# Kernel tuning notes

Measured on AMD Instinct MI355X. Metric: run time of the kernel, lower is better.

## Reference

```python
import jax, jax.numpy as jnp
import numpy as np

NEG_FILL = -10000000.0  # matches torch masked_fill value


def setup_inputs() -> dict:
    key = jax.random.key(0)
    kq, kk, kv = jax.random.split(key, 3)
    B, H, S, D = 4, 16, 2048, 64
    Q = jax.random.normal(kq, (B, H, S, D), dtype=jnp.float32)
    K = jax.random.normal(kk, (B, H, S, D), dtype=jnp.float32)
    V = jax.random.normal(kv, (B, H, S, D), dtype=jnp.float32)
    return {"Q": Q, "K": K, "V": V}


def reference(Q, K, V):
    # Q,K,V: [B,H,S,D]
    D = K.shape[-1]
    scale = 1.0 / jnp.sqrt(jnp.asarray(D, dtype=Q.dtype))
    # scores: [B,H,S,S]
    scores = jnp.einsum("bhqd,bhkd->bhqk", Q, K) * scale
    S = scores.shape[-1]
    # causal mask: True above diagonal (future positions) -> filled with NEG_FILL
    causal = jnp.triu(jnp.ones((S, S), dtype=bool), k=1)
    scores = jnp.where(causal, jnp.asarray(NEG_FILL, dtype=scores.dtype), scores)
    attn = jax.nn.softmax(scores, axis=-1)
    return jnp.einsum("bhqk,bhkd->bhqd", attn, V)
```

## Files before the change

kernel.cpp:

```cpp
#include <hip/hip_runtime.h>
#include <hip/hip_bf16.h>


#define SEQ 2048
#define DIM 64
#define BH  64

typedef _Float16 half8  __attribute__((ext_vector_type(8)));
typedef _Float16 half4v __attribute__((ext_vector_type(4)));
typedef float    float4v __attribute__((ext_vector_type(4)));
typedef unsigned short ushort4v __attribute__((ext_vector_type(4)));

__device__ __forceinline__ void async16(const _Float16* g, _Float16* l) {
    __builtin_amdgcn_global_load_lds(
        (const __attribute__((address_space(1))) void*)g,
        (__attribute__((address_space(3))) void*)l, 16, 0, 0);
}

#if defined(__has_builtin)
#if __has_builtin(__builtin_elementwise_min)
#define EMIN4(a, b) __builtin_elementwise_min((a), (b))
#endif
#if __has_builtin(__builtin_amdgcn_exp2f)
#define EXP2F(x) __builtin_amdgcn_exp2f(x)
#endif
#endif
#ifndef EMIN4
__device__ __forceinline__ half4v emin4_fallback(half4v a, half4v b) {
    half4v r;
    r[0] = a[0] < b[0] ? a[0] : b[0];
    r[1] = a[1] < b[1] ? a[1] : b[1];
    r[2] = a[2] < b[2] ? a[2] : b[2];
    r[3] = a[3] < b[3] ? a[3] : b[3];
    return r;
}
#define EMIN4(a, b) emin4_fallback((a), (b))
#endif
#ifndef EXP2F
#define EXP2F(x) exp2f(x)
#endif

__global__ __launch_bounds__(256)
void prep_kernel(const float* __restrict__ K, const float* __restrict__ V,
                 _Float16* __restrict__ Kh, _Float16* __restrict__ Vt) {
    const int bid = blockIdx.x;
    const int tid = threadIdx.x;
    if (bid < 4096) {
        size_t idx = (size_t)bid * 2048 + (size_t)tid * 8;
        float4v a = *(const float4v*)(K + idx);
        float4v b = *(const float4v*)(K + idx + 4);
        half8 h;
        h[0] = (_Float16)a[0]; h[1] = (_Float16)a[1];
        h[2] = (_Float16)a[2]; h[3] = (_Float16)a[3];
        h[4] = (_Float16)b[0]; h[5] = (_Float16)b[1];
        h[6] = (_Float16)b[2]; h[7] = (_Float16)b[3];
        *(half8*)(Kh + idx) = h;
    } else {
        __shared__ _Float16 Vl[64 * 64];
        const int b  = bid - 4096;
        const int bh = b >> 5;
        const int s0 = (b & 31) * 64;
        {
            const int r   = tid >> 2;
            const int c16 = (tid & 3) * 16;
            const float* p = V + ((size_t)bh * SEQ + s0 + r) * DIM + c16;
            float4v x0 = *(const float4v*)(p);
            float4v x1 = *(const float4v*)(p + 4);
            float4v x2 = *(const float4v*)(p + 8);
            float4v x3 = *(const float4v*)(p + 12);
            half8 h0, h1;
            h0[0] = (_Float16)x0[0]; h0[1] = (_Float16)x0[1];
            h0[2] = (_Float16)x0[2]; h0[3] = (_Float16)x0[3];
            h0[4] = (_Float16)x1[0]; h0[5] = (_Float16)x1[1];
            h0[6] = (_Float16)x1[2]; h0[7] = (_Float16)x1[3];
            h1[0] = (_Float16)x2[0]; h1[1] = (_Float16)x2[1];
            h1[2] = (_Float16)x2[2]; h1[3] = (_Float16)x2[3];
            h1[4] = (_Float16)x3[0]; h1[5] = (_Float16)x3[1];
            h1[6] = (_Float16)x3[2]; h1[7] = (_Float16)x3[3];
            const int k  = (r + (r >> 3)) & 7;
            const int j0 = c16 >> 3;
            *(half8*)&Vl[r * 64 + ((j0    ) ^ k) * 8] = h0;
            *(half8*)&Vl[r * 64 + ((j0 + 1) ^ k) * 8] = h1;
        }
        __syncthreads();
        {
            const int d  = tid >> 2;
            const int sc = (tid & 3) * 16;
            const int dh = d >> 3;
            const int dl = d & 7;
            half8 o0, o1;
#pragma unroll
            for (int j = 0; j < 8; ++j) {
                const int s1 = sc + j;
                const int s2 = sc + 8 + j;
                o0[j] = Vl[s1 * 64 + ((dh ^ ((s1 + (s1 >> 3)) & 7)) << 3) + dl];
                o1[j] = Vl[s2 * 64 + ((dh ^ ((s2 + (s2 >> 3)) & 7)) << 3) + dl];
            }
            _Float16* op = Vt + ((size_t)bh * DIM + d) * SEQ + s0 + sc;
            *(half8*)op       = o0;
            *(half8*)(op + 8) = o1;
        }
    }
}

__global__ __launch_bounds__(128, 2)
void fa_main(const float* __restrict__ Q, const _Float16* __restrict__ Kh,
             const _Float16* __restrict__ Vt, float* __restrict__ O) {
    const int bid = blockIdx.x;
    const int xcd = bid & 7;
    const int idx = bid >> 3;
    const int bh  = xcd * 8 + (idx & 7);
    const int t   = 31 - (idx >> 3);

    const float*    Qb = Q  + (size_t)bh * SEQ * DIM;
    const _Float16* Kb = Kh + (size_t)bh * SEQ * DIM;
    const _Float16* Vb = Vt + (size_t)bh * DIM * SEQ;
    float*          Ob = O  + (size_t)bh * SEQ * DIM;

    const int tid  = threadIdx.x;
    const int wave = tid >> 6;
    const int lane = tid & 63;
    const int row  = lane & 15;
    const int quad = lane >> 4;

    __shared__ _Float16 Kl[2][64 * 64];
    __shared__ _Float16 Vl[64 * 64];
    __shared__ _Float16 Pl[2][32 * 64];

    const float SC = 0.125f * 1.44269504f;
    const float4v z0 = {0.f, 0.f, 0.f, 0.f};
    half8 ones;
    {
        ushort4v ob;
        ob[0] = 0x3c00; ob[1] = 0x3c00; ob[2] = 0x3c00; ob[3] = 0x3c00;
        half4v o1 = __builtin_bit_cast(half4v, ob);
        ones[0] = o1[0]; ones[1] = o1[1]; ones[2] = o1[2]; ones[3] = o1[3];
        ones[4] = o1[0]; ones[5] = o1[1]; ones[6] = o1[2]; ones[7] = o1[3];
    }
    half4v wcap;
    {
        ushort4v cb2;
        cb2[0] = 0x7400; cb2[1] = 0x7400; cb2[2] = 0x7400; cb2[3] = 0x7400;
        wcap = __builtin_bit_cast(half4v, cb2);
    }

#define STAGE_K(bsel, kt_)                                                      \
    {                                                                           \
        const _Float16* Kt0 = Kb + (size_t)(kt_) * 64 * DIM;                    \
        _Pragma("unroll")                                                       \
        for (int i = 0; i < 4; ++i) {                                           \
            int pos = wave * 256 + i * 64 + lane;                               \
            int rr  = pos >> 3;                                                 \
            int cc  = (pos & 7) ^ (rr & 7);                                     \
            async16(Kt0 + (size_t)rr * DIM + cc * 8,                            \
                    &Kl[bsel][0] + (size_t)(wave * 256 + i * 64) * 8);          \
        }                                                                       \
    }
#define STAGE_V(kt_)                                                            \
    {                                                                           \
        const _Float16* Vt0 = Vb + (size_t)(kt_) * 64;                          \
        _Pragma("unroll")                                                       \
        for (int i = 0; i < 4; ++i) {                                           \
            int pos = wave * 256 + i * 64 + lane;                               \
            int rr  = pos >> 3;                                                 \
            int cc  = (pos & 7) ^ (rr & 7);                                     \
            async16(Vt0 + (size_t)rr * SEQ + cc * 8,                            \
                    &Vl[0] + (size_t)(wave * 256 + i * 64) * 8);                \
        }                                                                       \
    }

    const int q0 = t * 64;

    half8 qf[4];
#pragma unroll
    for (int qs = 0; qs < 2; ++qs) {
        const float* qp = Qb + (size_t)(q0 + wave * 32 + qs * 16 + row) * DIM;
#pragma unroll
        for (int s = 0; s < 2; ++s) {
            const float* p = qp + s * 32 + quad * 8;
            float4v a = *(const float4v*)p;
            float4v b = *(const float4v*)(p + 4);
            half8 h;
            h[0] = (_Float16)(a[0] * SC); h[1] = (_Float16)(a[1] * SC);
            h[2] = (_Float16)(a[2] * SC); h[3] = (_Float16)(a[3] * SC);
            h[4] = (_Float16)(b[0] * SC); h[5] = (_Float16)(b[1] * SC);
            h[6] = (_Float16)(b[2] * SC); h[7] = (_Float16)(b[3] * SC);
            qf[qs * 2 + s] = h;
        }
    }

    float4v o_acc[2][4];
    float4v lacc[2];
#pragma unroll
    for (int qs = 0; qs < 2; ++qs) {
        float4v z = {0.f, 0.f, 0.f, 0.f};
        lacc[qs] = z;
#pragma unroll
        for (int c = 0; c < 4; ++c) o_acc[qs][c] = z;
    }

    STAGE_K(0, 0)
    __syncthreads();

    for (int kt = 0; kt <= t; ++kt) {
        const int cb = kt & 1;
        STAGE_V(kt)
        if (kt < t) STAGE_K(cb ^ 1, kt + 1)

        float4v sacc[2][4];
        __builtin_amdgcn_s_setprio(1);
#pragma unroll
        for (int c = 0; c < 4; ++c) {
            const int kv  = c * 16 + row;
            const int ch0 = quad ^ (row & 7);
            const int ch1 = (4 + quad) ^ (row & 7);
            half8 kf0 = *(const half8*)&Kl[cb][kv * 64 + ch0 * 8];
            half8 kf1 = *(const half8*)&Kl[cb][kv * 64 + ch1 * 8];
#pragma unroll
            for (int qs = 0; qs < 2; ++qs) {
                float4v s0 = __builtin_amdgcn_mfma_f32_16x16x32_f16(kf0, qf[qs * 2 + 0], z0, 0, 0, 0);
                sacc[qs][c] = __builtin_amdgcn_mfma_f32_16x16x32_f16(kf1, qf[qs * 2 + 1], s0, 0, 0, 0);
            }
        }
        __builtin_amdgcn_s_setprio(0);

        float pv[2][4][4];
        if (kt == t) {
#pragma unroll
            for (int qs = 0; qs < 2; ++qs) {
                const int ql = wave * 32 + qs * 16 + row;
#pragma unroll
                for (int c = 0; c < 4; ++c)
#pragma unroll
                    for (int rr = 0; rr < 4; ++rr) {
                        int kvl = c * 16 + quad * 4 + rr;
                        float sx = (kvl > ql) ? -1e30f : sacc[qs][c][rr];
                        pv[qs][c][rr] = EXP2F(sx);
                    }
            }
        } else {
#pragma unroll
            for (int qs = 0; qs < 2; ++qs)
#pragma unroll
                for (int c = 0; c < 4; ++c)
#pragma unroll
                    for (int rr = 0; rr < 4; ++rr)
                        pv[qs][c][rr] = EXP2F(sacc[qs][c][rr]);
        }

#pragma unroll
        for (int qs = 0; qs < 2; ++qs)
#pragma unroll
            for (int c = 0; c < 4; ++c) {
#if defined(__has_builtin) && __has_builtin(__builtin_amdgcn_cvt_pkrtz)
                auto t0 = __builtin_amdgcn_cvt_pkrtz(pv[qs][c][0], pv[qs][c][1]);
                auto t1 = __builtin_amdgcn_cvt_pkrtz(pv[qs][c][2], pv[qs][c][3]);
                half4v w;
                w[0] = t0[0]; w[1] = t0[1]; w[2] = t1[0]; w[3] = t1[1];
#else
                half4v w;
                w[0] = (_Float16)pv[qs][c][0]; w[1] = (_Float16)pv[qs][c][1];
                w[2] = (_Float16)pv[qs][c][2]; w[3] = (_Float16)pv[qs][c][3];
#endif
                w = EMIN4(w, wcap);
                const int jc  = c * 2 + (quad >> 1);
                const int col = ((jc ^ (row & 7)) << 3) + (quad & 1) * 4;
                *(half4v*)&Pl[wave][(qs * 16 + row) * 64 + col] = w;
            }
        asm volatile("s_waitcnt lgkmcnt(0)" ::: "memory");
        half8 af[2][2];
#pragma unroll
        for (int qs = 0; qs < 2; ++qs)
#pragma unroll
            for (int s = 0; s < 2; ++s) {
                const int js = (s * 4 + quad) ^ (row & 7);
                af[qs][s] = *(const half8*)&Pl[wave][(qs * 16 + row) * 64 + js * 8];
            }

        if (kt < t) {
            asm volatile("s_waitcnt vmcnt(4)" ::: "memory");
        } else {
            asm volatile("s_waitcnt vmcnt(0)" ::: "memory");
        }
        __builtin_amdgcn_s_barrier();
        __builtin_amdgcn_sched_barrier(0);

        __builtin_amdgcn_s_setprio(1);
#pragma unroll
        for (int c = 0; c < 4; ++c) {
            const int d = c * 16 + row;
#pragma unroll
            for (int s = 0; s < 2; ++s) {
                const int ch = (s * 4 + quad) ^ (row & 7);
                half8 vf = *(const half8*)&Vl[d * 64 + ch * 8];
                o_acc[0][c] = __builtin_amdgcn_mfma_f32_16x16x32_f16(vf, af[0][s], o_acc[0][c], 0, 0, 0);
                o_acc[1][c] = __builtin_amdgcn_mfma_f32_16x16x32_f16(vf, af[1][s], o_acc[1][c], 0, 0, 0);
            }
        }
#pragma unroll
        for (int qs = 0; qs < 2; ++qs)
#pragma unroll
            for (int s = 0; s < 2; ++s)
                lacc[qs] = __builtin_amdgcn_mfma_f32_16x16x32_f16(ones, af[qs][s], lacc[qs], 0, 0, 0);
        __builtin_amdgcn_s_setprio(0);

        __syncthreads();
    }

#pragma unroll
    for (int qs = 0; qs < 2; ++qs) {
        const float inv = 1.0f / lacc[qs][0];
        float* op = Ob + (size_t)(q0 + wave * 32 + qs * 16 + row) * DIM + quad * 4;
#pragma unroll
        for (int c = 0; c < 4; ++c) {
            float4v o;
            o[0] = o_acc[qs][c][0] * inv; o[1] = o_acc[qs][c][1] * inv;
            o[2] = o_acc[qs][c][2] * inv; o[3] = o_acc[qs][c][3] * inv;
            *(float4v*)(op + c * 16) = o;
        }
    }
}

__global__ __launch_bounds__(256)
void fa_causal_fallback(const float* __restrict__ Q, const float* __restrict__ K,
                        const float* __restrict__ V, float* __restrict__ O) {
    const int bid = blockIdx.x;
    const int bh  = bid >> 5;
    const int qt  = bid & 31;
    const int q0  = qt * 64;

    const float* Qb = Q + (size_t)bh * SEQ * DIM;
    const float* Kb = K + (size_t)bh * SEQ * DIM;
    const float* Vb = V + (size_t)bh * SEQ * DIM;
    float*       Ob = O + (size_t)bh * SEQ * DIM;

    const int tid  = threadIdx.x;
    const int wave = tid >> 6;
    const int lane = tid & 63;
    const int row  = lane & 15;
    const int quad = lane >> 4;

    __shared__ _Float16 Kl[64][72];
    __shared__ _Float16 Vt[64][72];
    __shared__ _Float16 Pl[4][16][72];

    half8 qf[2];
    {
        const float* qp = Qb + (size_t)(q0 + wave * 16 + row) * DIM;
#pragma unroll
        for (int s = 0; s < 2; ++s) {
            const float* p = qp + s * 32 + quad * 8;
            float4v a = *(const float4v*)p;
            float4v b = *(const float4v*)(p + 4);
            half8 h;
            h[0] = (_Float16)a[0]; h[1] = (_Float16)a[1];
            h[2] = (_Float16)a[2]; h[3] = (_Float16)a[3];
            h[4] = (_Float16)b[0]; h[5] = (_Float16)b[1];
            h[6] = (_Float16)b[2]; h[7] = (_Float16)b[3];
            qf[s] = h;
        }
    }

    float m_i[4] = {-1e30f, -1e30f, -1e30f, -1e30f};
    float l_i[4] = {0.f, 0.f, 0.f, 0.f};
    float4v o_acc[4];
#pragma unroll
    for (int c = 0; c < 4; ++c) { float4v z = {0.f, 0.f, 0.f, 0.f}; o_acc[c] = z; }

    const float LOG2E = 1.44269504f;

    for (int kt = 0; kt <= qt; ++kt) {
        __syncthreads();
        {
            const int kvr = tid >> 2;
            const int c4  = tid & 3;
            const float* kp = Kb + (size_t)(kt * 64 + kvr) * DIM + c4 * 16;
            const float* vp = Vb + (size_t)(kt * 64 + kvr) * DIM + c4 * 16;
#pragma unroll
            for (int i = 0; i < 4; ++i) {
                float4v kx = *(const float4v*)(kp + i * 4);
                float4v vx = *(const float4v*)(vp + i * 4);
#pragma unroll
                for (int j = 0; j < 4; ++j) {
                    Kl[kvr][c4 * 16 + i * 4 + j] = (_Float16)kx[j];
                    Vt[c4 * 16 + i * 4 + j][kvr] = (_Float16)vx[j];
                }
            }
        }
        __syncthreads();

        float4v sacc[4];
#pragma unroll
        for (int c = 0; c < 4; ++c) { float4v z = {0.f, 0.f, 0.f, 0.f}; sacc[c] = z; }
#pragma unroll
        for (int c = 0; c < 4; ++c)
#pragma unroll
            for (int s = 0; s < 2; ++s) {
                half8 kf = *(const half8*)&Kl[c * 16 + row][s * 32 + quad * 8];
                sacc[c] = __builtin_amdgcn_mfma_f32_16x16x32_f16(qf[s], kf, sacc[c], 0, 0, 0);
            }

        float sv[4][4];
        const bool diag = (kt == qt);
#pragma unroll
        for (int c = 0; c < 4; ++c)
#pragma unroll
            for (int r = 0; r < 4; ++r) {
                float v = sacc[c][r] * 0.125f;
                if (diag) {
                    int kvl = c * 16 + row;
                    int ql  = wave * 16 + quad * 4 + r;
                    if (kvl > ql) v = -1e30f;
                }
                sv[c][r] = v;
            }

        float mnew[4], alpha[4];
#pragma unroll
        for (int r = 0; r < 4; ++r) {
            float rm = fmaxf(fmaxf(sv[0][r], sv[1][r]), fmaxf(sv[2][r], sv[3][r]));
            rm = fmaxf(rm, __shfl_xor(rm, 1));
            rm = fmaxf(rm, __shfl_xor(rm, 2));
            rm = fmaxf(rm, __shfl_xor(rm, 4));
            rm = fmaxf(rm, __shfl_xor(rm, 8));
            mnew[r]  = fmaxf(m_i[r], rm);
            alpha[r] = exp2f((m_i[r] - mnew[r]) * LOG2E);
            m_i[r]   = mnew[r];
        }
        float rs[4] = {0.f, 0.f, 0.f, 0.f};
#pragma unroll
        for (int c = 0; c < 4; ++c)
#pragma unroll
            for (int r = 0; r < 4; ++r) {
                float p = exp2f((sv[c][r] - mnew[r]) * LOG2E);
                sv[c][r] = p;
                rs[r] += p;
            }
#pragma unroll
        for (int r = 0; r < 4; ++r) {
            float s = rs[r];
            s += __shfl_xor(s, 1);
            s += __shfl_xor(s, 2);
            s += __shfl_xor(s, 4);
            s += __shfl_xor(s, 8);
            l_i[r] = l_i[r] * alpha[r] + s;
        }
#pragma unroll
        for (int c = 0; c < 4; ++c)
#pragma unroll
            for (int r = 0; r < 4; ++r)
                o_acc[c][r] *= alpha[r];

#pragma unroll
        for (int c = 0; c < 4; ++c)
#pragma unroll
            for (int r = 0; r < 4; ++r)
                Pl[wave][quad * 4 + r][c * 16 + row] = (_Float16)sv[c][r];
        __syncthreads();

        half8 af[2];
#pragma unroll
        for (int s = 0; s < 2; ++s)
            af[s] = *(const half8*)&Pl[wave][row][s * 32 + quad * 8];
#pragma unroll
        for (int c = 0; c < 4; ++c)
#pragma unroll
            for (int s = 0; s < 2; ++s) {
                half8 vf = *(const half8*)&Vt[c * 16 + row][s * 32 + quad * 8];
                o_acc[c] = __builtin_amdgcn_mfma_f32_16x16x32_f16(af[s], vf, o_acc[c], 0, 0, 0);
            }
    }

#pragma unroll
    for (int r = 0; r < 4; ++r) {
        float inv = 1.0f / l_i[r];
        float* op = Ob + (size_t)(q0 + wave * 16 + quad * 4 + r) * DIM;
#pragma unroll
        for (int c = 0; c < 4; ++c)
            op[c * 16 + row] = o_acc[c][r] * inv;
    }
}

extern "C" void kernel_launch(void* const* d_in, const int* in_sizes, int n_in,
                              void* d_out, int out_size, void* d_ws, size_t ws_size,
                              hipStream_t stream) {
    const float* Q = (const float*)d_in[0];
    const float* K = (const float*)d_in[1];
    const float* V = (const float*)d_in[2];
    float* O = (float*)d_out;

    const size_t elems = (size_t)BH * SEQ * DIM;
    const size_t need  = 2 * elems * sizeof(_Float16);

    if (ws_size >= need) {
        _Float16* Kh = (_Float16*)d_ws;
        _Float16* Vt = Kh + elems;
        prep_kernel<<<4096 + 2048, 256, 0, stream>>>(K, V, Kh, Vt);
        fa_main<<<BH * 32, 128, 0, stream>>>(Q, Kh, Vt, O);
    } else {
        fa_causal_fallback<<<BH * 32, 256, 0, stream>>>(Q, K, V, O);
    }
}
```

Before: 184.7 us.

## Use single-wave blocks with 32x32 tiles and barrier-free software pipeline

Shrinks each attention block to one wavefront covering 32 queries, with 32-key K/V tiles. The grid doubles to 4096 blocks. Block-wide barriers are replaced by explicit vmcnt waits around a prefetch schedule that stages the next V and the next-but-one K tile after the PV step. The diagonal tile gets its own specialized iteration. This is meant to remove barrier stalls, shrink shared memory for higher occupancy, and cut wasted causal work at finer granularity. The cost is that K/V tiles are no longer shared between two waves, so global/L2 traffic per query roughly doubles.

```diff
diff --git a/kernel.cpp b/kernel.cpp
--- a/kernel.cpp
+++ b/kernel.cpp
@@ -103,29 +103,27 @@
     }
 }
 
-__global__ __launch_bounds__(128, 2)
+__global__ __launch_bounds__(64, 2)
 void fa_main(const float* __restrict__ Q, const _Float16* __restrict__ Kh,
              const _Float16* __restrict__ Vt, float* __restrict__ O) {
     const int bid = blockIdx.x;
     const int xcd = bid & 7;
     const int idx = bid >> 3;
     const int bh  = xcd * 8 + (idx & 7);
-    const int t   = 31 - (idx >> 3);
+    const int t   = 63 - (idx >> 3);
 
     const float*    Qb = Q  + (size_t)bh * SEQ * DIM;
     const _Float16* Kb = Kh + (size_t)bh * SEQ * DIM;
     const _Float16* Vb = Vt + (size_t)bh * DIM * SEQ;
     float*          Ob = O  + (size_t)bh * SEQ * DIM;
 
-    const int tid  = threadIdx.x;
-    const int wave = tid >> 6;
-    const int lane = tid & 63;
+    const int lane = threadIdx.x;
     const int row  = lane & 15;
     const int quad = lane >> 4;
 
-    __shared__ _Float16 Kl[2][64 * 64];
-    __shared__ _Float16 Vl[64 * 64];
-    __shared__ _Float16 Pl[2][32 * 64];
+    __shared__ _Float16 Kl[2][32 * 64];
+    __shared__ _Float16 Vl[64 * 32];
+    __shared__ _Float16 Pl[32 * 64];
 
     const float SC = 0.125f * 1.44269504f;
     const float4v z0 = {0.f, 0.f, 0.f, 0.f};
@@ -146,35 +144,35 @@
 
 #define STAGE_K(bsel, kt_)                                                      \
     {                                                                           \
-        const _Float16* Kt0 = Kb + (size_t)(kt_) * 64 * DIM;                    \
+        const _Float16* Kt0 = Kb + (size_t)(kt_) * 32 * DIM;                    \
         _Pragma("unroll")                                                       \
         for (int i = 0; i < 4; ++i) {                                           \
-            int pos = wave * 256 + i * 64 + lane;                               \
+            int pos = i * 64 + lane;                                            \
             int rr  = pos >> 3;                                                 \
             int cc  = (pos & 7) ^ (rr & 7);                                     \
             async16(Kt0 + (size_t)rr * DIM + cc * 8,                            \
-                    &Kl[bsel][0] + (size_t)(wave * 256 + i * 64) * 8);          \
+                    &Kl[bsel][0] + (size_t)pos * 8);                            \
         }                                                                       \
     }
 #define STAGE_V(kt_)                                                            \
     {                                                                           \
-        const _Float16* Vt0 = Vb + (size_t)(kt_) * 64;                          \
+        const _Float16* Vt0 = Vb + (size_t)(kt_) * 32;                          \
         _Pragma("unroll")                                                       \
         for (int i = 0; i < 4; ++i) {                                           \
-            int pos = wave * 256 + i * 64 + lane;                               \
-            int rr  = pos >> 3;                                                 \
-            int cc  = (pos & 7) ^ (rr & 7);                                     \
+            int pos = i * 64 + lane;                                            \
+            int rr  = pos >> 2;                                                 \
+            int cc  = (pos & 3) ^ (rr & 3);                                     \
             async16(Vt0 + (size_t)rr * SEQ + cc * 8,                            \
-                    &Vl[0] + (size_t)(wave * 256 + i * 64) * 8);                \
-        }                                                                       \
-    }
-
-    const int q0 = t * 64;
+                    &Vl[0] + (size_t)pos * 8);                                  \
+        }                                                                       \
+    }
+
+    const int q0 = t * 32;
 
     half8 qf[4];
 #pragma unroll
     for (int qs = 0; qs < 2; ++qs) {
-        const float* qp = Qb + (size_t)(q0 + wave * 32 + qs * 16 + row) * DIM;
+        const float* qp = Qb + (size_t)(q0 + qs * 16 + row) * DIM;
 #pragma unroll
         for (int s = 0; s < 2; ++s) {
             const float* p = qp + s * 32 + quad * 8;
@@ -200,117 +198,106 @@
     }
 
     STAGE_K(0, 0)
-    __syncthreads();
-
-    for (int kt = 0; kt <= t; ++kt) {
-        const int cb = kt & 1;
-        STAGE_V(kt)
-        if (kt < t) STAGE_K(cb ^ 1, kt + 1)
-
-        float4v sacc[2][4];
-        __builtin_amdgcn_s_setprio(1);
-#pragma unroll
-        for (int c = 0; c < 4; ++c) {
-            const int kv  = c * 16 + row;
-            const int ch0 = quad ^ (row & 7);
-            const int ch1 = (4 + quad) ^ (row & 7);
-            half8 kf0 = *(const half8*)&Kl[cb][kv * 64 + ch0 * 8];
-            half8 kf1 = *(const half8*)&Kl[cb][kv * 64 + ch1 * 8];
-#pragma unroll
-            for (int qs = 0; qs < 2; ++qs) {
-                float4v s0 = __builtin_amdgcn_mfma_f32_16x16x32_f16(kf0, qf[qs * 2 + 0], z0, 0, 0, 0);
-                sacc[qs][c] = __builtin_amdgcn_mfma_f32_16x16x32_f16(kf1, qf[qs * 2 + 1], s0, 0, 0, 0);
-            }
-        }
-        __builtin_amdgcn_s_setprio(0);
-
-        float pv[2][4][4];
-        if (kt == t) {
-#pragma unroll
-            for (int qs = 0; qs < 2; ++qs) {
-                const int ql = wave * 32 + qs * 16 + row;
-#pragma unroll
-                for (int c = 0; c < 4; ++c)
-#pragma unroll
-                    for (int rr = 0; rr < 4; ++rr) {
-                        int kvl = c * 16 + quad * 4 + rr;
-                        float sx = (kvl > ql) ? -1e30f : sacc[qs][c][rr];
-                        pv[qs][c][rr] = EXP2F(sx);
-                    }
-            }
-        } else {
-#pragma unroll
-            for (int qs = 0; qs < 2; ++qs)
-#pragma unroll
-                for (int c = 0; c < 4; ++c)
-#pragma unroll
-                    for (int rr = 0; rr < 4; ++rr)
-                        pv[qs][c][rr] = EXP2F(sacc[qs][c][rr]);
-        }
-
-#pragma unroll
-        for (int qs = 0; qs < 2; ++qs)
-#pragma unroll
-            for (int c = 0; c < 4; ++c) {
-#if defined(__has_builtin) && __has_builtin(__builtin_amdgcn_cvt_pkrtz)
-                auto t0 = __builtin_amdgcn_cvt_pkrtz(pv[qs][c][0], pv[qs][c][1]);
-                auto t1 = __builtin_amdgcn_cvt_pkrtz(pv[qs][c][2], pv[qs][c][3]);
-                half4v w;
-                w[0] = t0[0]; w[1] = t0[1]; w[2] = t1[0]; w[3] = t1[1];
-#else
-                half4v w;
-                w[0] = (_Float16)pv[qs][c][0]; w[1] = (_Float16)pv[qs][c][1];
-                w[2] = (_Float16)pv[qs][c][2]; w[3] = (_Float16)pv[qs][c][3];
-#endif
-                w = EMIN4(w, wcap);
-                const int jc  = c * 2 + (quad >> 1);
-                const int col = ((jc ^ (row & 7)) << 3) + (quad & 1) * 4;
-                *(half4v*)&Pl[wave][(qs * 16 + row) * 64 + col] = w;
-            }
-        asm volatile("s_waitcnt lgkmcnt(0)" ::: "memory");
-        half8 af[2][2];
-#pragma unroll
-        for (int qs = 0; qs < 2; ++qs)
-#pragma unroll
-            for (int s = 0; s < 2; ++s) {
-                const int js = (s * 4 + quad) ^ (row & 7);
-                af[qs][s] = *(const half8*)&Pl[wave][(qs * 16 + row) * 64 + js * 8];
-            }
-
-        if (kt < t) {
-            asm volatile("s_waitcnt vmcnt(4)" ::: "memory");
-        } else {
-            asm volatile("s_waitcnt vmcnt(0)" ::: "memory");
-        }
-        __builtin_amdgcn_s_barrier();
-        __builtin_amdgcn_sched_barrier(0);
-
-        __builtin_amdgcn_s_setprio(1);
-#pragma unroll
-        for (int c = 0; c < 4; ++c) {
-            const int d = c * 16 + row;
-#pragma unroll
-            for (int s = 0; s < 2; ++s) {
-                const int ch = (s * 4 + quad) ^ (row & 7);
-                half8 vf = *(const half8*)&Vl[d * 64 + ch * 8];
-                o_acc[0][c] = __builtin_amdgcn_mfma_f32_16x16x32_f16(vf, af[0][s], o_acc[0][c], 0, 0, 0);
-                o_acc[1][c] = __builtin_amdgcn_mfma_f32_16x16x32_f16(vf, af[1][s], o_acc[1][c], 0, 0, 0);
-            }
-        }
-#pragma unroll
-        for (int qs = 0; qs < 2; ++qs)
-#pragma unroll
-            for (int s = 0; s < 2; ++s)
-                lacc[qs] = __builtin_amdgcn_mfma_f32_16x16x32_f16(ones, af[qs][s], lacc[qs], 0, 0, 0);
-        __builtin_amdgcn_s_setprio(0);
-
-        __syncthreads();
-    }
+    STAGE_V(0)
+    if (t >= 1) STAGE_K(1, 1)
+
+#define KV_ITER(kt_, DIAG, STV, STK)                                            \
+    {                                                                           \
+        const int cb = (kt_) & 1;                                               \
+        if (DIAG) { asm volatile("s_waitcnt vmcnt(4)" ::: "memory"); }          \
+        else      { asm volatile("s_waitcnt vmcnt(8)" ::: "memory"); }          \
+        __builtin_amdgcn_sched_barrier(0);                                      \
+                                           \
+        float4v sacc[2][2];                                                     \
+        __builtin_amdgcn_s_setprio(1);                                          \
+        _Pragma("unroll")                                                       \
+        for (int c = 0; c < 2; ++c) {                                           \
+            const int kv  = c * 16 + row;                                       \
+            const int ch0 = quad ^ (kv & 7);                                    \
+            const int ch1 = (4 + quad) ^ (kv & 7);                              \
+            half8 kf0 = *(const half8*)&Kl[cb][kv * 64 + ch0 * 8];              \
+            half8 kf1 = *(const half8*)&Kl[cb][kv * 64 + ch1 * 8];              \
+            _Pragma("unroll")                                                   \
+            for (int qs = 0; qs < 2; ++qs) {                                    \
+                float4v s0 = __builtin_amdgcn_mfma_f32_16x16x32_f16(            \
+                    kf0, qf[qs * 2 + 0], z0, 0, 0, 0);                          \
+                sacc[qs][c] = __builtin_amdgcn_mfma_f32_16x16x32_f16(           \
+                    kf1, qf[qs * 2 + 1], s0, 0, 0, 0);                          \
+            }                                                                   \
+        }                                                                       \
+        __builtin_amdgcn_s_setprio(0);                                          \
+                               \
+        _Pragma("unroll")                                                       \
+        for (int qs = 0; qs < 2; ++qs) {                                        \
+            const int ql = qs * 16 + row;                                       \
+            _Pragma("unroll")                                                   \
+            for (int c = 0; c < 2; ++c) {                                       \
+                float p0[4];                                                    \
+                _Pragma("unroll")                                               \
+                for (int rr = 0; rr < 4; ++rr) {                                \
+                    float sx = sacc[qs][c][rr];                                 \
+                    if (DIAG) {                                                 \
+                        int kvl = c * 16 + quad * 4 + rr;                       \
+                        sx = (kvl > ql) ? -1e30f : sx;                          \
+                    }                                                           \
+                    p0[rr] = EXP2F(sx);                                         \
+                }                                                               \
+                half4v w;                                                       \
+                {                                                               \
+                    auto t0_ = __builtin_amdgcn_cvt_pkrtz(p0[0], p0[1]);        \
+                    auto t1_ = __builtin_amdgcn_cvt_pkrtz(p0[2], p0[3]);        \
+                    w[0] = t0_[0]; w[1] = t0_[1]; w[2] = t1_[0]; w[3] = t1_[1]; \
+                }                                                               \
+                w = EMIN4(w, wcap);                                             \
+                const int jc  = c * 2 + (quad >> 1);                            \
+                const int col = ((jc ^ (row & 7)) << 3) + (quad & 1) * 4;       \
+                *(half4v*)&Pl[(qs * 16 + row) * 64 + col] = w;                  \
+            }                                                                   \
+        }                                                                       \
+        asm volatile("s_waitcnt lgkmcnt(0)" ::: "memory");                      \
+        half8 af[2];                                                            \
+        {                                                                       \
+            const int js = quad ^ (row & 7);                                    \
+            af[0] = *(const half8*)&Pl[(row) * 64 + js * 8];                    \
+            af[1] = *(const half8*)&Pl[(16 + row) * 64 + js * 8];               \
+        }                                                                       \
+                 \
+        if (DIAG) { asm volatile("s_waitcnt vmcnt(0)" ::: "memory"); }          \
+        else      { asm volatile("s_waitcnt vmcnt(4)" ::: "memory"); }          \
+        __builtin_amdgcn_sched_barrier(0);                                      \
+                                        \
+        __builtin_amdgcn_s_setprio(1);                                          \
+        _Pragma("unroll")                                                       \
+        for (int c = 0; c < 4; ++c) {                                           \
+            const int d  = c * 16 + row;                                        \
+            const int ch = quad ^ (d & 3);                                      \
+            half8 vf = *(const half8*)&Vl[d * 32 + ch * 8];                     \
+            o_acc[0][c] = __builtin_amdgcn_mfma_f32_16x16x32_f16(               \
+                vf, af[0], o_acc[0][c], 0, 0, 0);                               \
+            o_acc[1][c] = __builtin_amdgcn_mfma_f32_16x16x32_f16(               \
+                vf, af[1], o_acc[1][c], 0, 0, 0);                               \
+        }                                                                       \
+        lacc[0] = __builtin_amdgcn_mfma_f32_16x16x32_f16(ones, af[0], lacc[0], 0, 0, 0); \
+        lacc[1] = __builtin_amdgcn_mfma_f32_16x16x32_f16(ones, af[1], lacc[1], 0, 0, 0); \
+        __builtin_amdgcn_s_setprio(0);                                          \
+        if (!(DIAG)) {                                                          \
+               \
+            asm volatile("s_waitcnt lgkmcnt(0)" ::: "memory");                  \
+            __builtin_amdgcn_sched_barrier(0);                                  \
+            if (STV) STAGE_V((kt_) + 1)                                         \
+            if (STK) STAGE_K(cb, (kt_) + 2)                                     \
+        }                                                                       \
+    }
+
+    for (int kt = 0; kt < t; ++kt) {
+        KV_ITER(kt, false, true, (kt < t - 1))
+    }
+    KV_ITER(t, true, false, false)
 
 #pragma unroll
     for (int qs = 0; qs < 2; ++qs) {
         const float inv = 1.0f / lacc[qs][0];
-        float* op = Ob + (size_t)(q0 + wave * 32 + qs * 16 + row) * DIM + quad * 4;
+        float* op = Ob + (size_t)(q0 + qs * 16 + row) * DIM + quad * 4;
 #pragma unroll
         for (int c = 0; c < 4; ++c) {
             float4v o;
@@ -496,7 +483,7 @@
         _Float16* Kh = (_Float16*)d_ws;
         _Float16* Vt = Kh + elems;
         prep_kernel<<<4096 + 2048, 256, 0, stream>>>(K, V, Kh, Vt);
-        fa_main<<<BH * 32, 128, 0, stream>>>(Q, Kh, Vt, O);
+        fa_main<<<BH * 64, 64, 0, stream>>>(Q, Kh, Vt, O);
     } else {
         fa_causal_fallback<<<BH * 32, 256, 0, stream>>>(Q, K, V, O);
     }
```

New measurement: 194.5 us. 5.3% more time.

## Pair complementary causal query tiles per block with one 64-row tile per wave

Applied to the files above, without the earlier changes.

Each block now handles two query tiles, pr and 31-pr, one per wave, with each wave covering 64 query rows. Both waves share the K/V tiles staged for the longer tile, and the wave with the shorter tile sits idle after its diagonal. This balances the causal triangle across blocks and halves the grid to 1024 blocks. K is now double-buffered two tiles ahead with reordered waits and barriers. The cost is twice the accumulator registers per wave, half the blocks, and one idle wave for part of each loop.

```diff
diff --git a/kernel.cpp b/kernel.cpp
--- a/kernel.cpp
+++ b/kernel.cpp
@@ -108,9 +108,10 @@
              const _Float16* __restrict__ Vt, float* __restrict__ O) {
     const int bid = blockIdx.x;
     const int xcd = bid & 7;
-    const int idx = bid >> 3;
-    const int bh  = xcd * 8 + (idx & 7);
-    const int t   = 31 - (idx >> 3);
+    const int g   = (bid >> 3) & 31;
+    const int sw  = bid >> 8;
+    const int bh  = xcd * 8 + (g & 7);
+    const int pr  = (g >> 3) + sw * 4;
 
     const float*    Qb = Q  + (size_t)bh * SEQ * DIM;
     const _Float16* Kb = Kh + (size_t)bh * SEQ * DIM;
@@ -123,9 +124,13 @@
     const int row  = lane & 15;
     const int quad = lane >> 4;
 
+    const int t_w  = wave ? (31 - pr) : pr;
+    const int maxT = 31 - pr;
+    const int q0w  = t_w * 64;
+
     __shared__ _Float16 Kl[2][64 * 64];
     __shared__ _Float16 Vl[64 * 64];
-    __shared__ _Float16 Pl[2][32 * 64];
+    __shared__ _Float16 Pl[2][64 * 64];
 
     const float SC = 0.125f * 1.44269504f;
     const float4v z0 = {0.f, 0.f, 0.f, 0.f};
@@ -169,15 +174,13 @@
         }                                                                       \
     }
 
-    const int q0 = t * 64;
-
-    half8 qf[4];
-#pragma unroll
-    for (int qs = 0; qs < 2; ++qs) {
-        const float* qp = Qb + (size_t)(q0 + wave * 32 + qs * 16 + row) * DIM;
-#pragma unroll
-        for (int s = 0; s < 2; ++s) {
-            const float* p = qp + s * 32 + quad * 8;
+    half8 qf[4][2];
+#pragma unroll
+    for (int qs = 0; qs < 4; ++qs) {
+        const float* qp = Qb + (size_t)(q0w + qs * 16 + row) * DIM;
+#pragma unroll
+        for (int s2 = 0; s2 < 2; ++s2) {
+            const float* p = qp + s2 * 32 + quad * 8;
             float4v a = *(const float4v*)p;
             float4v b = *(const float4v*)(p + 4);
             half8 h;
@@ -185,14 +188,14 @@
             h[2] = (_Float16)(a[2] * SC); h[3] = (_Float16)(a[3] * SC);
             h[4] = (_Float16)(b[0] * SC); h[5] = (_Float16)(b[1] * SC);
             h[6] = (_Float16)(b[2] * SC); h[7] = (_Float16)(b[3] * SC);
-            qf[qs * 2 + s] = h;
-        }
-    }
-
-    float4v o_acc[2][4];
-    float4v lacc[2];
-#pragma unroll
-    for (int qs = 0; qs < 2; ++qs) {
+            qf[qs][s2] = h;
+        }
+    }
+
+    float4v o_acc[4][4];
+    float4v lacc[4];
+#pragma unroll
+    for (int qs = 0; qs < 4; ++qs) {
         float4v z = {0.f, 0.f, 0.f, 0.f};
         lacc[qs] = z;
 #pragma unroll
@@ -200,117 +203,113 @@
     }
 
     STAGE_K(0, 0)
-    __syncthreads();
-
-    for (int kt = 0; kt <= t; ++kt) {
+    STAGE_K(1, 1)
+
+    for (int kt = 0; kt <= maxT; ++kt) {
         const int cb = kt & 1;
+        if (kt == maxT) { asm volatile("s_waitcnt vmcnt(0)" ::: "memory"); }
+        else           { asm volatile("s_waitcnt vmcnt(4)" ::: "memory"); }
+        __builtin_amdgcn_sched_barrier(0);
+        __builtin_amdgcn_s_barrier();
         STAGE_V(kt)
-        if (kt < t) STAGE_K(cb ^ 1, kt + 1)
-
-        float4v sacc[2][4];
-        __builtin_amdgcn_s_setprio(1);
-#pragma unroll
-        for (int c = 0; c < 4; ++c) {
-            const int kv  = c * 16 + row;
-            const int ch0 = quad ^ (row & 7);
-            const int ch1 = (4 + quad) ^ (row & 7);
-            half8 kf0 = *(const half8*)&Kl[cb][kv * 64 + ch0 * 8];
-            half8 kf1 = *(const half8*)&Kl[cb][kv * 64 + ch1 * 8];
-#pragma unroll
-            for (int qs = 0; qs < 2; ++qs) {
-                float4v s0 = __builtin_amdgcn_mfma_f32_16x16x32_f16(kf0, qf[qs * 2 + 0], z0, 0, 0, 0);
-                sacc[qs][c] = __builtin_amdgcn_mfma_f32_16x16x32_f16(kf1, qf[qs * 2 + 1], s0, 0, 0, 0);
-            }
-        }
-        __builtin_amdgcn_s_setprio(0);
-
-        float pv[2][4][4];
-        if (kt == t) {
-#pragma unroll
-            for (int qs = 0; qs < 2; ++qs) {
-                const int ql = wave * 32 + qs * 16 + row;
-#pragma unroll
-                for (int c = 0; c < 4; ++c)
+
+        const bool act = (kt <= t_w);
+        half8 af[4][2];
+        if (act) {
+            float4v sacc[4][4];
+            __builtin_amdgcn_s_setprio(1);
+#pragma unroll
+            for (int c = 0; c < 4; ++c) {
+                const int kv  = c * 16 + row;
+                const int ch0 = quad ^ (row & 7);
+                const int ch1 = (4 + quad) ^ (row & 7);
+                half8 kf0 = *(const half8*)&Kl[cb][kv * 64 + ch0 * 8];
+                half8 kf1 = *(const half8*)&Kl[cb][kv * 64 + ch1 * 8];
+#pragma unroll
+                for (int qs = 0; qs < 4; ++qs) {
+                    float4v s0 = __builtin_amdgcn_mfma_f32_16x16x32_f16(kf0, qf[qs][0], z0, 0, 0, 0);
+                    sacc[qs][c] = __builtin_amdgcn_mfma_f32_16x16x32_f16(kf1, qf[qs][1], s0, 0, 0, 0);
+                }
+            }
+            __builtin_amdgcn_s_setprio(0);
+
+            const bool dg = (kt == t_w);
+#pragma unroll
+            for (int qs = 0; qs < 4; ++qs) {
+                const int ql = qs * 16 + row;
+#pragma unroll
+                for (int c = 0; c < 4; ++c) {
+                    float p0[4];
 #pragma unroll
                     for (int rr = 0; rr < 4; ++rr) {
-                        int kvl = c * 16 + quad * 4 + rr;
-                        float sx = (kvl > ql) ? -1e30f : sacc[qs][c][rr];
-                        pv[qs][c][rr] = EXP2F(sx);
+                        float sx = sacc[qs][c][rr];
+                        if (dg) {
+                            int kvl = c * 16 + quad * 4 + rr;
+                            sx = (kvl > ql) ? -1e30f : sx;
+                        }
+                        p0[rr] = EXP2F(sx);
                     }
-            }
-        } else {
-#pragma unroll
-            for (int qs = 0; qs < 2; ++qs)
-#pragma unroll
-                for (int c = 0; c < 4; ++c)
-#pragma unroll
-                    for (int rr = 0; rr < 4; ++rr)
-                        pv[qs][c][rr] = EXP2F(sacc[qs][c][rr]);
-        }
-
-#pragma unroll
-        for (int qs = 0; qs < 2; ++qs)
+#if defined(__has_builtin) && __has_builtin(__builtin_amdgcn_cvt_pkrtz)
+                    auto t0_ = __builtin_amdgcn_cvt_pkrtz(p0[0], p0[1]);
+                    auto t1_ = __builtin_amdgcn_cvt_pkrtz(p0[2], p0[3]);
+                    half4v w;
+                    w[0] = t0_[0]; w[1] = t0_[1]; w[2] = t1_[0]; w[3] = t1_[1];
+#else
+                    half4v w;
+                    w[0] = (_Float16)p0[0]; w[1] = (_Float16)p0[1];
+                    w[2] = (_Float16)p0[2]; w[3] = (_Float16)p0[3];
+#endif
+                    w = EMIN4(w, wcap);
+                    const int jc  = c * 2 + (quad >> 1);
+                    const int col = ((jc ^ (row & 7)) << 3) + (quad & 1) * 4;
+                    *(half4v*)&Pl[wave][(qs * 16 + row) * 64 + col] = w;
+                }
+            }
+        }
+        asm volatile("s_waitcnt lgkmcnt(0)" ::: "memory");
+        __builtin_amdgcn_sched_barrier(0);
+        if (act) {
+#pragma unroll
+            for (int qs = 0; qs < 4; ++qs)
+#pragma unroll
+                for (int s2 = 0; s2 < 2; ++s2) {
+                    const int js = (s2 * 4 + quad) ^ (row & 7);
+                    af[qs][s2] = *(const half8*)&Pl[wave][(qs * 16 + row) * 64 + js * 8];
+                }
+        }
+
+        asm volatile("s_waitcnt vmcnt(0)" ::: "memory");
+        __builtin_amdgcn_sched_barrier(0);
+        __builtin_amdgcn_s_barrier();
+        if (kt + 2 <= maxT) STAGE_K(cb, kt + 2)
+
+        if (act) {
+            __builtin_amdgcn_s_setprio(1);
 #pragma unroll
             for (int c = 0; c < 4; ++c) {
-#if defined(__has_builtin) && __has_builtin(__builtin_amdgcn_cvt_pkrtz)
-                auto t0 = __builtin_amdgcn_cvt_pkrtz(pv[qs][c][0], pv[qs][c][1]);
-                auto t1 = __builtin_amdgcn_cvt_pkrtz(pv[qs][c][2], pv[qs][c][3]);
-                half4v w;
-                w[0] = t0[0]; w[1] = t0[1]; w[2] = t1[0]; w[3] = t1[1];
-#else
-                half4v w;
-                w[0] = (_Float16)pv[qs][c][0]; w[1] = (_Float16)pv[qs][c][1];
-                w[2] = (_Float16)pv[qs][c][2]; w[3] = (_Float16)pv[qs][c][3];
-#endif
-                w = EMIN4(w, wcap);
-                const int jc  = c * 2 + (quad >> 1);
-                const int col = ((jc ^ (row & 7)) << 3) + (quad & 1) * 4;
-                *(half4v*)&Pl[wave][(qs * 16 + row) * 64 + col] = w;
-            }
-        asm volatile("s_waitcnt lgkmcnt(0)" ::: "memory");
-        half8 af[2][2];
-#pragma unroll
-        for (int qs = 0; qs < 2; ++qs)
-#pragma unroll
-            for (int s = 0; s < 2; ++s) {
-                const int js = (s * 4 + quad) ^ (row & 7);
-                af[qs][s] = *(const half8*)&Pl[wave][(qs * 16 + row) * 64 + js * 8];
-            }
-
-        if (kt < t) {
-            asm volatile("s_waitcnt vmcnt(4)" ::: "memory");
-        } else {
-            asm volatile("s_waitcnt vmcnt(0)" ::: "memory");
-        }
-        __builtin_amdgcn_s_barrier();
-        __builtin_amdgcn_sched_barrier(0);
-
-        __builtin_amdgcn_s_setprio(1);
-#pragma unroll
-        for (int c = 0; c < 4; ++c) {
-            const int d = c * 16 + row;
-#pragma unroll
-            for (int s = 0; s < 2; ++s) {
-                const int ch = (s * 4 + quad) ^ (row & 7);
-                half8 vf = *(const half8*)&Vl[d * 64 + ch * 8];
-                o_acc[0][c] = __builtin_amdgcn_mfma_f32_16x16x32_f16(vf, af[0][s], o_acc[0][c], 0, 0, 0);
-                o_acc[1][c] = __builtin_amdgcn_mfma_f32_16x16x32_f16(vf, af[1][s], o_acc[1][c], 0, 0, 0);
-            }
-        }
-#pragma unroll
-        for (int qs = 0; qs < 2; ++qs)
-#pragma unroll
-            for (int s = 0; s < 2; ++s)
-                lacc[qs] = __builtin_amdgcn_mfma_f32_16x16x32_f16(ones, af[qs][s], lacc[qs], 0, 0, 0);
-        __builtin_amdgcn_s_setprio(0);
-
-        __syncthreads();
-    }
-
-#pragma unroll
-    for (int qs = 0; qs < 2; ++qs) {
+                const int d = c * 16 + row;
+#pragma unroll
+                for (int s2 = 0; s2 < 2; ++s2) {
+                    const int ch = (s2 * 4 + quad) ^ (row & 7);
+                    half8 vf = *(const half8*)&Vl[d * 64 + ch * 8];
+#pragma unroll
+                    for (int qs = 0; qs < 4; ++qs)
+                        o_acc[qs][c] = __builtin_amdgcn_mfma_f32_16x16x32_f16(vf, af[qs][s2], o_acc[qs][c], 0, 0, 0);
+                }
+            }
+#pragma unroll
+            for (int qs = 0; qs < 4; ++qs)
+#pragma unroll
+                for (int s2 = 0; s2 < 2; ++s2)
+                    lacc[qs] = __builtin_amdgcn_mfma_f32_16x16x32_f16(ones, af[qs][s2], lacc[qs], 0, 0, 0);
+            __builtin_amdgcn_s_setprio(0);
+        }
+    }
+
+#pragma unroll
+    for (int qs = 0; qs < 4; ++qs) {
         const float inv = 1.0f / lacc[qs][0];
-        float* op = Ob + (size_t)(q0 + wave * 32 + qs * 16 + row) * DIM + quad * 4;
+        float* op = Ob + (size_t)(q0w + qs * 16 + row) * DIM + quad * 4;
 #pragma unroll
         for (int c = 0; c < 4; ++c) {
             float4v o;
@@ -496,7 +495,7 @@
         _Float16* Kh = (_Float16*)d_ws;
         _Float16* Vt = Kh + elems;
         prep_kernel<<<4096 + 2048, 256, 0, stream>>>(K, V, Kh, Vt);
-        fa_main<<<BH * 32, 128, 0, stream>>>(Q, Kh, Vt, O);
+        fa_main<<<1024, 128, 0, stream>>>(Q, Kh, Vt, O);
     } else {
         fa_causal_fallback<<<BH * 32, 256, 0, stream>>>(Q, K, V, O);
     }
```

After: 201.4 us. +9.1%, slower.

## Double-buffer V and prefetch K two tiles ahead, aliasing P into idle V buffer

Applied to the files above, without the earlier changes.

V is now double-buffered and the P scratch tile is aliased into the V buffer not in use, so LDS use stays about the same. Loads are issued further ahead: the V tile for step kt+1 and the K tile for step kt+2 are staged after the mid-iteration barrier. The trailing __syncthreads is replaced by a single vmcnt wait plus barrier at the top of each iteration. The goal is more overlap between global-to-LDS copies and MFMA work with fewer barriers. In exchange it relies on exact vmcnt counts and on P writes never overlapping V data still being read, and it issues redundant clamped loads on the last iterations.

```diff
diff --git a/kernel.cpp b/kernel.cpp
--- a/kernel.cpp
+++ b/kernel.cpp
@@ -124,8 +124,7 @@
     const int quad = lane >> 4;
 
     __shared__ _Float16 Kl[2][64 * 64];
-    __shared__ _Float16 Vl[64 * 64];
-    __shared__ _Float16 Pl[2][32 * 64];
+    __shared__ _Float16 Vl[2][64 * 64];
 
     const float SC = 0.125f * 1.44269504f;
     const float4v z0 = {0.f, 0.f, 0.f, 0.f};
@@ -156,7 +155,7 @@
                     &Kl[bsel][0] + (size_t)(wave * 256 + i * 64) * 8);          \
         }                                                                       \
     }
-#define STAGE_V(kt_)                                                            \
+#define STAGE_V(bsel, kt_)                                                      \
     {                                                                           \
         const _Float16* Vt0 = Vb + (size_t)(kt_) * 64;                          \
         _Pragma("unroll")                                                       \
@@ -165,7 +164,7 @@
             int rr  = pos >> 3;                                                 \
             int cc  = (pos & 7) ^ (rr & 7);                                     \
             async16(Vt0 + (size_t)rr * SEQ + cc * 8,                            \
-                    &Vl[0] + (size_t)(wave * 256 + i * 64) * 8);                \
+                    &Vl[bsel][0] + (size_t)(wave * 256 + i * 64) * 8);          \
         }                                                                       \
     }
 
@@ -200,12 +199,17 @@
     }
 
     STAGE_K(0, 0)
-    __syncthreads();
+    STAGE_V(0, 0)
+    STAGE_K(1, (1 <= t ? 1 : t))
 
     for (int kt = 0; kt <= t; ++kt) {
         const int cb = kt & 1;
-        STAGE_V(kt)
-        if (kt < t) STAGE_K(cb ^ 1, kt + 1)
+        _Float16* Pw = &Vl[cb ^ 1][wave * 2048];
+
+        asm volatile("s_waitcnt vmcnt(8)" ::: "memory");
+        __builtin_amdgcn_s_barrier();
+        __builtin_amdgcn_sched_barrier(0);
+        asm volatile("" ::: "memory");
 
         float4v sacc[2][4];
         __builtin_amdgcn_s_setprio(1);
@@ -265,7 +269,7 @@
                 w = EMIN4(w, wcap);
                 const int jc  = c * 2 + (quad >> 1);
                 const int col = ((jc ^ (row & 7)) << 3) + (quad & 1) * 4;
-                *(half4v*)&Pl[wave][(qs * 16 + row) * 64 + col] = w;
+                *(half4v*)&Pw[(qs * 16 + row) * 64 + col] = w;
             }
         asm volatile("s_waitcnt lgkmcnt(0)" ::: "memory");
         half8 af[2][2];
@@ -274,16 +278,20 @@
 #pragma unroll
             for (int s = 0; s < 2; ++s) {
                 const int js = (s * 4 + quad) ^ (row & 7);
-                af[qs][s] = *(const half8*)&Pl[wave][(qs * 16 + row) * 64 + js * 8];
-            }
-
-        if (kt < t) {
-            asm volatile("s_waitcnt vmcnt(4)" ::: "memory");
-        } else {
-            asm volatile("s_waitcnt vmcnt(0)" ::: "memory");
-        }
+                af[qs][s] = *(const half8*)&Pw[(qs * 16 + row) * 64 + js * 8];
+            }
+
+        asm volatile("s_waitcnt vmcnt(4)" ::: "memory");
         __builtin_amdgcn_s_barrier();
         __builtin_amdgcn_sched_barrier(0);
+        asm volatile("s_waitcnt lgkmcnt(0)" ::: "memory");
+
+        {
+            const int vn = (kt + 1 <= t) ? kt + 1 : t;
+            const int kn = (kt + 2 <= t) ? kt + 2 : t;
+            STAGE_V(cb ^ 1, vn)
+            STAGE_K(cb, kn)
+        }
 
         __builtin_amdgcn_s_setprio(1);
 #pragma unroll
@@ -292,7 +300,7 @@
 #pragma unroll
             for (int s = 0; s < 2; ++s) {
                 const int ch = (s * 4 + quad) ^ (row & 7);
-                half8 vf = *(const half8*)&Vl[d * 64 + ch * 8];
+                half8 vf = *(const half8*)&Vl[cb][d * 64 + ch * 8];
                 o_acc[0][c] = __builtin_amdgcn_mfma_f32_16x16x32_f16(vf, af[0][s], o_acc[0][c], 0, 0, 0);
                 o_acc[1][c] = __builtin_amdgcn_mfma_f32_16x16x32_f16(vf, af[1][s], o_acc[1][c], 0, 0, 0);
             }
@@ -303,8 +311,6 @@
             for (int s = 0; s < 2; ++s)
                 lacc[qs] = __builtin_amdgcn_mfma_f32_16x16x32_f16(ones, af[qs][s], lacc[qs], 0, 0, 0);
         __builtin_amdgcn_s_setprio(0);
-
-        __syncthreads();
     }
 
 #pragma unroll
```

New measurement: 185.5 us. About the same (+0.5%).
